# Kernel optimization log

Hardware: AMD Instinct MI355X
Metric: run time of the kernel (lower is better)

## Reference

```python
import jax, jax.numpy as jnp
import numpy as np

T, N, E, D, OUT, L = 12, 10000, 160000, 128, 64, 2


def setup_inputs() -> dict:
    key = jax.random.key(0)
    ks = jax.random.split(key, 8)
    s = 1.0 / np.sqrt(D)
    x = jax.random.normal(ks[0], (T, N, D), jnp.float32)
    hidden_states = jax.random.normal(ks[1], (L, N, D), jnp.float32)
    src = jax.random.randint(ks[2], (E,), 0, N, dtype=jnp.int32)
    dst = jax.random.randint(ks[3], (E,), 0, N, dtype=jnp.int32)
    W_self = jax.random.normal(ks[4], (L, 6, D, D), jnp.float32) * s
    W_neigh = jax.random.normal(ks[5], (L, 6, D, D), jnp.float32) * s
    b = jnp.zeros((L, 6, D), jnp.float32)
    W_out = jax.random.normal(ks[6], (D, OUT), jnp.float32) * s
    b_out = jnp.zeros((OUT,), jnp.float32)
    return dict(x=x, hidden_states=hidden_states, W_self=W_self, W_neigh=W_neigh,
                b=b, W_out=W_out, b_out=b_out, src=src, dst=dst)


def reference(x, hidden_states, W_self, W_neigh, b, W_out, b_out, src, dst):
    n_nodes = x.shape[1]
    deg = jax.ops.segment_sum(jnp.ones_like(dst, jnp.float32), dst, num_segments=n_nodes)
    deg_inv = jnp.where(deg > 0, 1.0 / deg, 0.0)[:, None]  # [N,1]

    def agg(f):  # mean over in-neighbors (DGL update_all copy_u + mean)
        return jax.ops.segment_sum(f[src], dst, num_segments=n_nodes) * deg_inv

    # agg_seq=True: original concatenates all timesteps and does one update_all;
    # mean is per-feature, so this equals per-timestep neighbor means, vmapped.
    hN_all = jax.vmap(agg)(x)  # [T,N,D]

    def net(f, fN, i, Ws, Wn, bl):  # SAGE-mean style message-passing net
        return f @ Ws[i] + fN @ Wn[i] + bl[i]

    def cell(xin, h, hN_x, Ws, Wn, bl):
        if hN_x is None:
            hN_x = agg(xin)
        hN_h = agg(h)
        r = jax.nn.sigmoid(net(xin, hN_x, 0, Ws, Wn, bl) + net(h, hN_h, 1, Ws, Wn, bl))
        u = jax.nn.sigmoid(net(xin, hN_x, 2, Ws, Wn, bl) + net(h, hN_h, 3, Ws, Wn, bl))
        c = jnp.tanh(net(xin, hN_x, 4, Ws, Wn, bl) + net(h, hN_h, 5, Ws, Wn, bl))
        return u * h + (1.0 - u) * c  # note: r*h is dead code in the source

    def step(hidden, inp_t):
        x_t, hN_t = inp_t
        cur, hN = x_t, hN_t
        new_h = []
        for j in range(L):  # small fixed depth
            cur = cell(cur, hidden[j], hN, W_self[j], W_neigh[j], b[j])
            new_h.append(cur)
            hN = None  # h_N only used by first layer (as in source)
        out = cur @ W_out + b_out
        return jnp.stack(new_h), out

    hidden_final, outputs = jax.lax.scan(step, hidden_states, (x, hN_all))
    return outputs, hidden_final
```

## Files before the change

### kernel.cpp

```cpp
#include <hip/hip_runtime.h>

typedef unsigned short u16;
typedef unsigned int   u32;
typedef __attribute__((ext_vector_type(4))) float f32x4;
typedef __attribute__((ext_vector_type(8))) short s16x8;

#define TT 12
#define NN 10000
#define EE 160000
#define DD 128
#define OO 64

__device__ __forceinline__ u16 f2bf(float f) {
  union { float f; u32 u; } x; x.f = f;
  u32 r = x.u + 0x7FFFu + ((x.u >> 16) & 1u);
  return (u16)(r >> 16);
}
__device__ __forceinline__ float bf2f(u16 v) {
  union { u32 u; float f; } x; x.u = (u32)v << 16; return x.f;
}

__global__ __launch_bounds__(256) void prep_kernel(
    const float* __restrict__ x, const float* __restrict__ hs,
    const int* __restrict__ dst,
    const float* __restrict__ Wself, const float* __restrict__ Wneigh,
    const float* __restrict__ b, const float* __restrict__ Wout,
    u16* __restrict__ xb, float* __restrict__ h0f, u16* __restrict__ hb0,
    float* __restrict__ h1f, u16* __restrict__ hb1,
    int* __restrict__ deg, u16* __restrict__ Wp,
    float* __restrict__ biasbuf, u16* __restrict__ WoT,
    int nx4, int nh4half, int E) {
  int gid = blockIdx.x * 256 + threadIdx.x;
  const int NWP = 2 * 256 * 512;
  int cvtEnd  = nx4 + 2 * nh4half;
  int cntEnd  = cvtEnd + E;
  if (gid < nx4) {
    float4 v = *(const float4*)(x + (size_t)gid * 4);
    uint2 p;
    p.x = (u32)f2bf(v.x) | ((u32)f2bf(v.y) << 16);
    p.y = (u32)f2bf(v.z) | ((u32)f2bf(v.w) << 16);
    *(uint2*)(xb + (size_t)gid * 4) = p;
  } else if (gid < cvtEnd) {
    int j = gid - nx4;
    int half = (j >= nh4half);
    int jj = half ? j - nh4half : j;
    float4 v = ((const float4*)hs)[j];
    float* fdst = half ? h1f : h0f;
    u16*   bdst = half ? hb1 : hb0;
    ((float4*)fdst)[jj] = v;
    uint2 p;
    p.x = (u32)f2bf(v.x) | ((u32)f2bf(v.y) << 16);
    p.y = (u32)f2bf(v.z) | ((u32)f2bf(v.w) << 16);
    ((uint2*)bdst)[jj] = p;
  } else if (gid < cntEnd) {
    int e = gid - cvtEnd;
    atomicAdd(&deg[dst[e]], 1);
  } else {
    int pg = gid - cntEnd;
    if (pg < NWP) {
      int j = pg >> 17;
      int rem = pg & 131071;
      int c = rem >> 9;
      int k = rem & 511;
      int seg = k >> 7, kd = k & 127;
      int cc = c & 127;
      int gate = (c < 128) ? (seg < 2 ? 2 : 3) : (seg < 2 ? 4 : 5);
      const float* M = (seg & 1) ? Wneigh : Wself;
      float v = M[((j * 6 + gate) * 128 + kd) * 128 + cc];
      Wp[pg] = f2bf(v);
    } else if (pg < NWP + 64 * 128) {
      int i = pg - NWP;
      int c = i >> 7, k = i & 127;
      WoT[i] = f2bf(Wout[k * OO + c]);
    } else if (pg < NWP + 64 * 128 + 512) {
      int i = pg - NWP - 64 * 128;
      int j = i >> 8, g = (i >> 7) & 1, d = i & 127;
      int g1 = g ? 4 : 2, g2 = g ? 5 : 3;
      biasbuf[i] = b[(j * 6 + g1) * 128 + d] + b[(j * 6 + g2) * 128 + d];
    }
  }
}

__global__ __launch_bounds__(1024) void scan_kernel(const int* __restrict__ deg,
                                                    int* __restrict__ offs,
                                                    float* __restrict__ dinv, int n) {
  __shared__ int lds_deg[10240];
  __shared__ int wsum[16];
  int tid = threadIdx.x;
  for (int i = tid; i < 10240; i += 1024) lds_deg[i] = (i < n) ? deg[i] : 0;
  __syncthreads();
  int base = tid * 10;
  int loc[10];
  int s = 0;
  #pragma unroll
  for (int k = 0; k < 10; ++k) { loc[k] = s; s += lds_deg[base + k]; }
  int lane = tid & 63;
  int incl = s;
  #pragma unroll
  for (int d = 1; d < 64; d <<= 1) {
    int t2 = __shfl_up(incl, d);
    if (lane >= d) incl += t2;
  }
  int wid = tid >> 6;
  if (lane == 63) wsum[wid] = incl;
  __syncthreads();
  int wpre = 0;
  for (int k = 0; k < wid; ++k) wpre += wsum[k];
  int excl = wpre + incl - s;
  #pragma unroll
  for (int k = 0; k < 10; ++k) {
    int idx = base + k;
    if (idx < n) {
      int d0 = lds_deg[idx];
      offs[idx] = excl + loc[k];
      dinv[idx] = (d0 > 0) ? 1.0f / (float)d0 : 0.0f;
    }
  }
  if (tid == 1023) offs[n] = excl + s;
}

__global__ __launch_bounds__(256) void fill_kernel(const int* __restrict__ src,
                                                   const int* __restrict__ dst,
                                                   const int* __restrict__ offs,
                                                   int* __restrict__ cursor,
                                                   int* __restrict__ csr, int E) {
  int e = blockIdx.x * 256 + threadIdx.x;
  if (e >= E) return;
  int d = dst[e];
  int pos = atomicAdd(&cursor[d], 1);
  csr[offs[d] + pos] = src[e] * 64;
}

__device__ __forceinline__ void agg_one(const int* __restrict__ offs,
                                        const int* __restrict__ csr,
                                        const float* __restrict__ dinv,
                                        const u32* __restrict__ S,
                                        u32* __restrict__ O,
                                        int node, int lane) {
  int nu = __builtin_amdgcn_readfirstlane(node);
  int e0 = offs[nu], e1 = offs[nu + 1];
  float di = dinv[nu];
  float xa = 0.f, ya = 0.f, xb_ = 0.f, yb_ = 0.f;
  float xc = 0.f, yc = 0.f, xd = 0.f, yd = 0.f;
  int e = e0;
  for (; e + 8 <= e1; e += 8) {
    int i0 = csr[e],     i1 = csr[e + 1], i2 = csr[e + 2], i3 = csr[e + 3];
    int i4 = csr[e + 4], i5 = csr[e + 5], i6 = csr[e + 6], i7 = csr[e + 7];
    u32 v0 = S[i0 + lane], v1 = S[i1 + lane], v2 = S[i2 + lane], v3 = S[i3 + lane];
    u32 v4 = S[i4 + lane], v5 = S[i5 + lane], v6 = S[i6 + lane], v7 = S[i7 + lane];
    xa  += bf2f((u16)v0) + bf2f((u16)v1);
    ya  += bf2f((u16)(v0 >> 16)) + bf2f((u16)(v1 >> 16));
    xb_ += bf2f((u16)v2) + bf2f((u16)v3);
    yb_ += bf2f((u16)(v2 >> 16)) + bf2f((u16)(v3 >> 16));
    xc  += bf2f((u16)v4) + bf2f((u16)v5);
    yc  += bf2f((u16)(v4 >> 16)) + bf2f((u16)(v5 >> 16));
    xd  += bf2f((u16)v6) + bf2f((u16)v7);
    yd  += bf2f((u16)(v6 >> 16)) + bf2f((u16)(v7 >> 16));
  }
  for (; e + 4 <= e1; e += 4) {
    int i0 = csr[e], i1 = csr[e + 1], i2 = csr[e + 2], i3 = csr[e + 3];
    u32 v0 = S[i0 + lane], v1 = S[i1 + lane], v2 = S[i2 + lane], v3 = S[i3 + lane];
    xa  += bf2f((u16)v0) + bf2f((u16)v1);
    ya  += bf2f((u16)(v0 >> 16)) + bf2f((u16)(v1 >> 16));
    xb_ += bf2f((u16)v2) + bf2f((u16)v3);
    yb_ += bf2f((u16)(v2 >> 16)) + bf2f((u16)(v3 >> 16));
  }
  for (; e < e1; ++e) {
    u32 v = S[csr[e] + lane];
    xa += bf2f((u16)v); ya += bf2f((u16)(v >> 16));
  }
  float sx = ((xa + xb_) + (xc + xd)) * di;
  float sy = ((ya + yb_) + (yc + yd)) * di;
  O[nu * 64 + lane] = (u32)f2bf(sx) | ((u32)f2bf(sy) << 16);
}

__global__ __launch_bounds__(256) void aggs_kernel(const int* __restrict__ offs,
                                                   const int* __restrict__ csr,
                                                   const float* __restrict__ dinv,
                                                   const u16* __restrict__ s,
                                                   u16* __restrict__ o, int N) {
  int node = blockIdx.x * 4 + (threadIdx.x >> 6);
  if (node >= N) return;
  agg_one(offs, csr, dinv, (const u32*)s, (u32*)o, node, threadIdx.x & 63);
}

__global__ __launch_bounds__(256) void aggx_kernel(const int* __restrict__ offs,
                                                   const int* __restrict__ csr,
                                                   const float* __restrict__ dinv,
                                                   const u16* __restrict__ xb,
                                                   u16* __restrict__ axb, int N) {
  int id = blockIdx.x;
  int t, grp;
  if (id < 20000) {
    t = id & 7;
    grp = id >> 3;
  } else {
    int j = id - 20000;
    int slot = j & 7;
    t = 8 + (slot & 3);
    grp = (slot >> 2) * 1250 + (j >> 3);
  }
  int node = grp * 4 + (threadIdx.x >> 6);
  if (node >= N) return;
  size_t yo = (size_t)t * N * 64;
  agg_one(offs, csr, dinv, (const u32*)xb + yo, (u32*)axb + yo, node, threadIdx.x & 63);
}

__global__ __launch_bounds__(256) void aggdual_kernel(const int* __restrict__ offs,
                                                      const int* __restrict__ csr,
                                                      const float* __restrict__ dinv,
                                                      const u16* __restrict__ s0,
                                                      const u16* __restrict__ s1,
                                                      u16* __restrict__ o0,
                                                      u16* __restrict__ o1, int N) {
  int b = blockIdx.x;
  int srcsel = (b >> 2) & 1;
  int idx = (b >> 3) * 4 + (b & 3);
  int node = idx * 4 + (threadIdx.x >> 6);
  if (node >= N) return;
  const u32* S = (const u32*)(srcsel ? s1 : s0);
  u32* O = (u32*)(srcsel ? o1 : o0);
  agg_one(offs, csr, dinv, S, O, node, threadIdx.x & 63);
}

template <int MODE>
__device__ __forceinline__ void cell_body(char* __restrict__ smem, int row0, int tid,
    const u16* __restrict__ s0, const u16* __restrict__ s1,
    const u16* __restrict__ s2, const u16* __restrict__ s3,
    const u16* __restrict__ W, const float* __restrict__ bias,
    float* __restrict__ P,
    const float* __restrict__ hin, float* __restrict__ hout, u16* __restrict__ hbout,
    const u16* __restrict__ WoT, const float* __restrict__ bout,
    float* __restrict__ outp, int N) {
  constexpr int NKC = (MODE == 2) ? 8 : 4;
  u16* As = (u16*)smem;
  u16* Bs = (u16*)(smem + 8192);
  const u16* srcs[4] = {s0, s1, s2, s3};
  int lane = tid & 63, w = tid >> 6;
  int wr = w & 3, wc = w >> 2;

  f32x4 accU[4], accC[4];
  if constexpr (MODE == 1) {
    #pragma unroll
    for (int n = 0; n < 4; ++n) {
      int col = wc * 64 + n * 16 + (lane & 15);
      #pragma unroll
      for (int r = 0; r < 4; ++r) {
        int row = row0 + wr * 16 + (lane >> 4) * 4 + r;
        accU[n][r] = (row < N) ? P[(size_t)row * 256 + col] : 0.f;
        accC[n][r] = (row < N) ? P[(size_t)row * 256 + col + 128] : 0.f;
      }
    }
  } else {
    #pragma unroll
    for (int n = 0; n < 4; ++n) { accU[n] = (f32x4){0,0,0,0}; accC[n] = (f32x4){0,0,0,0}; }
  }

  #pragma unroll
  for (int kc = 0; kc < NKC; ++kc) {
    {
      int r = tid >> 3, k8 = (tid & 7) * 8;
      const u16* sp = srcs[kc >> 1];
      int grow = row0 + r;
      uint4 v = make_uint4(0, 0, 0, 0);
      if (grow < N) v = *(const uint4*)(sp + (size_t)grow * DD + (kc & 1) * 64 + k8);
      int byte = (r * 128 + (tid & 7) * 16) ^ ((r & 7) << 4);
      *(uint4*)((char*)As + byte) = v;
    }
    #pragma unroll
    for (int it = 0; it < 4; ++it) {
      int id = it * 512 + tid;
      int c = id >> 3, k8 = (id & 7) * 8;
      uint4 v = *(const uint4*)(W + c * 512 + kc * 64 + k8);
      int byte = (c * 128 + (id & 7) * 16) ^ ((c & 7) << 4);
      *(uint4*)((char*)Bs + byte) = v;
    }
    __syncthreads();
    #pragma unroll
    for (int ks = 0; ks < 2; ++ks) {
      int arow = wr * 16 + (lane & 15);
      int abyte = (arow * 128 + ks * 64 + (lane >> 4) * 16) ^ ((arow & 7) << 4);
      s16x8 af = *(const s16x8*)((char*)As + abyte);
      #pragma unroll
      for (int n = 0; n < 4; ++n) {
        int cu = wc * 64 + n * 16 + (lane & 15);
        int bub = (cu * 128 + ks * 64 + (lane >> 4) * 16) ^ ((cu & 7) << 4);
        s16x8 bu = *(const s16x8*)((char*)Bs + bub);
        accU[n] = __builtin_amdgcn_mfma_f32_16x16x32_bf16(af, bu, accU[n], 0, 0, 0);
        int cc = cu + 128;
        int bcb = (cc * 128 + ks * 64 + (lane >> 4) * 16) ^ ((cc & 7) << 4);
        s16x8 bc = *(const s16x8*)((char*)Bs + bcb);
        accC[n] = __builtin_amdgcn_mfma_f32_16x16x32_bf16(af, bc, accC[n], 0, 0, 0);
      }
    }
    __syncthreads();
  }

  if constexpr (MODE == 0) {
    #pragma unroll
    for (int n = 0; n < 4; ++n) {
      int col = wc * 64 + n * 16 + (lane & 15);
      #pragma unroll
      for (int r = 0; r < 4; ++r) {
        int row = row0 + wr * 16 + (lane >> 4) * 4 + r;
        if (row < N) {
          P[(size_t)row * 256 + col] = accU[n][r];
          P[(size_t)row * 256 + col + 128] = accC[n][r];
        }
      }
    }
  } else {
    #pragma unroll
    for (int n = 0; n < 4; ++n) {
      int col = wc * 64 + n * 16 + (lane & 15);
      float bu = bias[col], bc = bias[128 + col];
      #pragma unroll
      for (int r = 0; r < 4; ++r) {
        int row = row0 + wr * 16 + (lane >> 4) * 4 + r;
        if (row < N) {
          float u = 1.0f / (1.0f + __expf(-(accU[n][r] + bu)));
          float cg = tanhf(accC[n][r] + bc);
          size_t idx = (size_t)row * DD + col;
          float hn = u * hin[idx] + (1.0f - u) * cg;
          hout[idx] = hn;
          u16 hnb = f2bf(hn);
          hbout[idx] = hnb;
          if constexpr (MODE == 2) {
            int rl = row - row0;
            int hbyte = (rl * 256 + col * 2) ^ ((rl & 7) << 4);
            *(u16*)(smem + hbyte) = hnb;
          }
        }
      }
    }
    if constexpr (MODE == 2) {
      #pragma unroll
      for (int it = 0; it < 2; ++it) {
        int id = it * 512 + tid;
        int c = id >> 4, kc8 = (id & 15) * 8;
        uint4 v = *(const uint4*)(WoT + c * 128 + kc8);
        int byte = (c * 256 + kc8 * 2) ^ ((c & 7) << 4);
        *(uint4*)(smem + 16384 + byte) = v;
      }
      __syncthreads();
      f32x4 ao[2] = {};
      #pragma unroll
      for (int ks = 0; ks < 4; ++ks) {
        int arow = wr * 16 + (lane & 15);
        int abyte = (arow * 256 + ks * 64 + (lane >> 4) * 16) ^ ((arow & 7) << 4);
        s16x8 af = *(const s16x8*)(smem + abyte);
        #pragma unroll
        for (int n = 0; n < 2; ++n) {
          int co = wc * 32 + n * 16 + (lane & 15);
          int bbyte = (co * 256 + ks * 64 + (lane >> 4) * 16) ^ ((co & 7) << 4);
          s16x8 bf = *(const s16x8*)(smem + 16384 + bbyte);
          ao[n] = __builtin_amdgcn_mfma_f32_16x16x32_bf16(af, bf, ao[n], 0, 0, 0);
        }
      }
      #pragma unroll
      for (int n = 0; n < 2; ++n) {
        int co = wc * 32 + n * 16 + (lane & 15);
        float bb = bout[co];
        #pragma unroll
        for (int r = 0; r < 4; ++r) {
          int row = row0 + wr * 16 + (lane >> 4) * 4 + r;
          if (row < N) outp[(size_t)row * OO + co] = ao[n][r] + bb;
        }
      }
    }
  }
}

__global__ __launch_bounds__(512) void pre_kernel(const u16* __restrict__ xb,
                                                  const u16* __restrict__ axb,
                                                  const u16* __restrict__ Wp,
                                                  float* __restrict__ P, int N) {
  __shared__ __align__(16) char smem[40960];
  size_t yo = (size_t)blockIdx.y * N * DD;
  cell_body<0>(smem, blockIdx.x * 64, threadIdx.x, xb + yo, axb + yo, nullptr, nullptr,
               Wp, nullptr, P + (size_t)blockIdx.y * N * 256,
               nullptr, nullptr, nullptr, nullptr, nullptr, nullptr, N);
}

__global__ __launch_bounds__(512) void cell0_kernel(const u16* __restrict__ hb0c,
                                                    const u16* __restrict__ ah0,
                                                    const u16* __restrict__ W,
                                                    const float* __restrict__ bias,
                                                    float* __restrict__ Pt,
                                                    const float* __restrict__ h0in,
                                                    float* __restrict__ h0out,
                                                    u16* __restrict__ hb0out, int N) {
  __shared__ __align__(16) char smem[40960];
  cell_body<1>(smem, blockIdx.x * 64, threadIdx.x, hb0c, ah0, nullptr, nullptr,
               W, bias, Pt, h0in, h0out, hb0out, nullptr, nullptr, nullptr, N);
}

template <int WITHC0>
__global__ __launch_bounds__(512) void step_kernel(const u16* __restrict__ hb0c,
                                                   const u16* __restrict__ ah0,
                                                   const u16* __restrict__ hb1r,
                                                   const u16* __restrict__ ah1,
                                                   const u16* __restrict__ Wp,
                                                   const float* __restrict__ biasbuf,
                                                   float* __restrict__ Pn,
                                                   const float* __restrict__ h1in,
                                                   float* __restrict__ h1out,
                                                   u16* __restrict__ hb1w,
                                                   const float* __restrict__ h0in,
                                                   float* __restrict__ h0out,
                                                   u16* __restrict__ hb0out,
                                                   const u16* __restrict__ WoT,
                                                   const float* __restrict__ bout,
                                                   float* __restrict__ outp, int N) {
  __shared__ __align__(16) char smem[40960];
  int bx = blockIdx.x;
  int role = WITHC0 ? (bx & 1) : 0;
  int row0 = (WITHC0 ? (bx >> 1) : bx) * 64;
  if (role == 0) {
    cell_body<2>(smem, row0, threadIdx.x, hb0c, ah0, hb1r, ah1,
                 Wp + 131072, biasbuf + 256, nullptr,
                 h1in, h1out, hb1w, WoT, bout, outp, N);
  } else {
    cell_body<1>(smem, row0, threadIdx.x, hb0c, ah0, nullptr, nullptr,
                 Wp + 256, biasbuf, Pn,
                 h0in, h0out, hb0out, nullptr, nullptr, nullptr, N);
  }
}

extern "C" void kernel_launch(void* const* d_in, const int* in_sizes, int n_in,
                              void* d_out, int out_size, void* d_ws, size_t ws_size,
                              hipStream_t stream) {
  const float* x      = (const float*)d_in[0];
  const float* hs     = (const float*)d_in[1];
  const float* Wself  = (const float*)d_in[2];
  const float* Wneigh = (const float*)d_in[3];
  const float* b      = (const float*)d_in[4];
  const float* Wout   = (const float*)d_in[5];
  const float* bout   = (const float*)d_in[6];
  const int*   src    = (const int*)d_in[7];
  const int*   dst    = (const int*)d_in[8];
  float* out = (float*)d_out;

  const int N = NN, E = EE, D = DD, T = TT;

  char* ws = (char*)d_ws;
  size_t off = 0;
  auto alloc = [&](size_t bytes) -> void* {
    void* p = ws + off;
    off = (off + bytes + 255) & ~(size_t)255;
    return p;
  };
  int*   deg     = (int*)alloc(N * 4);
  int*   offs    = (int*)alloc((N + 1) * 4);
  int*   cursor  = (int*)alloc(N * 4);
  int*   csr     = (int*)alloc(E * 4);
  float* dinv    = (float*)alloc(N * 4);
  u16*   Wp      = (u16*)alloc(2 * 256 * 512 * 2);
  float* biasbuf = (float*)alloc(512 * 4);
  u16*   WoT     = (u16*)alloc(64 * 128 * 2);
  float* h0A     = (float*)alloc((size_t)N * D * 4);
  float* h0B     = (float*)alloc((size_t)N * D * 4);
  float* h1f     = (float*)alloc((size_t)N * D * 4);
  u16*   hb0A    = (u16*)alloc((size_t)N * D * 2);
  u16*   hb0B    = (u16*)alloc((size_t)N * D * 2);
  u16*   hb1     = (u16*)alloc((size_t)N * D * 2);
  u16*   ah0b    = (u16*)alloc((size_t)N * D * 2);
  u16*   ah1b    = (u16*)alloc((size_t)N * D * 2);
  u16*   xb      = (u16*)alloc((size_t)T * N * D * 2);
  u16*   axb     = (u16*)alloc((size_t)T * N * D * 2);
  float* P       = (float*)alloc((size_t)T * N * 256 * 4);

  float* h0f[2] = {h0A, h0B};
  u16*   hb0[2] = {hb0A, hb0B};
  float* hid0 = out + (size_t)T * N * OO;
  float* hid1 = hid0 + (size_t)N * D;

  hipMemsetAsync(deg, 0, N * 4, stream);
  hipMemsetAsync(cursor, 0, N * 4, stream);
  {
    int nx4 = T * N * D / 4, nh4half = N * D / 4;
    int tot = nx4 + 2 * nh4half + E + (2 * 256 * 512 + 64 * 128 + 512);
    prep_kernel<<<(tot + 255) / 256, 256, 0, stream>>>(
        x, hs, dst, Wself, Wneigh, b, Wout,
        xb, h0A, hb0A, h1f, hb1, deg, Wp, biasbuf, WoT, nx4, nh4half, E);
  }
  scan_kernel<<<1, 1024, 0, stream>>>(deg, offs, dinv, N);
  fill_kernel<<<(E + 255) / 256, 256, 0, stream>>>(src, dst, offs, cursor, csr, E);

  int aggGrid = (N + 3) / 4;
  int mmGrid  = (N + 63) / 64;

  aggx_kernel<<<30000, 256, 0, stream>>>(offs, csr, dinv, xb, axb, N);
  pre_kernel<<<dim3(mmGrid, T), 512, 0, stream>>>(xb, axb, Wp, P, N);
  aggs_kernel<<<aggGrid, 256, 0, stream>>>(offs, csr, dinv, hb0A, ah0b, N);
  cell0_kernel<<<mmGrid, 512, 0, stream>>>(hb0A, ah0b, Wp + 256, biasbuf, P,
                                           h0A, h0B, hb0B, N);

  for (int t = 0; t < T; ++t) {
    u16* cur = hb0[(t + 1) & 1];
    aggdual_kernel<<<2 * aggGrid, 256, 0, stream>>>(offs, csr, dinv, cur, hb1,
                                                    ah0b, ah1b, N);
    if (t < T - 1) {
      float* h0o = (t == T - 2) ? hid0 : h0f[t & 1];
      step_kernel<1><<<2 * mmGrid, 512, 0, stream>>>(
          cur, ah0b, hb1, ah1b, Wp, biasbuf,
          P + (size_t)(t + 1) * N * 256,
          h1f, h1f, hb1,
          h0f[(t + 1) & 1], h0o, hb0[t & 1],
          WoT, bout, out + (size_t)t * N * OO, N);
    } else {
      step_kernel<0><<<mmGrid, 512, 0, stream>>>(
          cur, ah0b, hb1, ah1b, Wp, biasbuf, nullptr,
          h1f, hid1, hb1, nullptr, nullptr, nullptr,
          WoT, bout, out + (size_t)t * N * OO, N);
    }
  }
}
```

Before: 681.0 us.

## Fuse layer-0 input projection into per-step cell kernel, drop precomputed P buffer

Removes the batched pre_kernel that computed x/agg(x) projections for all timesteps into a large fp32 P buffer. The layer-0 cell now runs a full K=512 GEMM over x, agg(x), h and agg(h) each step, so it no longer writes and rereads roughly 123 MB of fp32 partial sums. The prep kernel is also reordered to pack weights first and to convert 8 floats per thread. The trade-off is doubled per-step GEMM K-work for layer 0, which sits on the serial recurrent path, in exchange for removing the P memory traffic.

```diff
diff --git a/kernel.cpp b/kernel.cpp
--- a/kernel.cpp
+++ b/kernel.cpp
@@ -29,34 +29,15 @@
     float* __restrict__ h1f, u16* __restrict__ hb1,
     int* __restrict__ deg, u16* __restrict__ Wp,
     float* __restrict__ biasbuf, u16* __restrict__ WoT,
-    int nx4, int nh4half, int E) {
+    int nx8, int nh8half, int E) {
   int gid = blockIdx.x * 256 + threadIdx.x;
   const int NWP = 2 * 256 * 512;
-  int cvtEnd  = nx4 + 2 * nh4half;
-  int cntEnd  = cvtEnd + E;
-  if (gid < nx4) {
-    float4 v = *(const float4*)(x + (size_t)gid * 4);
-    uint2 p;
-    p.x = (u32)f2bf(v.x) | ((u32)f2bf(v.y) << 16);
-    p.y = (u32)f2bf(v.z) | ((u32)f2bf(v.w) << 16);
-    *(uint2*)(xb + (size_t)gid * 4) = p;
-  } else if (gid < cvtEnd) {
-    int j = gid - nx4;
-    int half = (j >= nh4half);
-    int jj = half ? j - nh4half : j;
-    float4 v = ((const float4*)hs)[j];
-    float* fdst = half ? h1f : h0f;
-    u16*   bdst = half ? hb1 : hb0;
-    ((float4*)fdst)[jj] = v;
-    uint2 p;
-    p.x = (u32)f2bf(v.x) | ((u32)f2bf(v.y) << 16);
-    p.y = (u32)f2bf(v.z) | ((u32)f2bf(v.w) << 16);
-    ((uint2*)bdst)[jj] = p;
-  } else if (gid < cntEnd) {
-    int e = gid - cvtEnd;
-    atomicAdd(&deg[dst[e]], 1);
-  } else {
-    int pg = gid - cntEnd;
+  const int NPACK = NWP + 64 * 128 + 512;
+  int cvtXEnd = NPACK + nx8;
+  int cvtHEnd = cvtXEnd + 2 * nh8half;
+  int cntEnd  = cvtHEnd + E;
+  if (gid < NPACK) {
+    int pg = gid;
     if (pg < NWP) {
       int j = pg >> 17;
       int rem = pg & 131071;
@@ -72,12 +53,41 @@
       int i = pg - NWP;
       int c = i >> 7, k = i & 127;
       WoT[i] = f2bf(Wout[k * OO + c]);
-    } else if (pg < NWP + 64 * 128 + 512) {
+    } else {
       int i = pg - NWP - 64 * 128;
       int j = i >> 8, g = (i >> 7) & 1, d = i & 127;
       int g1 = g ? 4 : 2, g2 = g ? 5 : 3;
       biasbuf[i] = b[(j * 6 + g1) * 128 + d] + b[(j * 6 + g2) * 128 + d];
     }
+  } else if (gid < cvtXEnd) {
+    int i8 = gid - NPACK;
+    float4 va = *(const float4*)(x + (size_t)i8 * 8);
+    float4 vb = *(const float4*)(x + (size_t)i8 * 8 + 4);
+    uint4 p;
+    p.x = (u32)f2bf(va.x) | ((u32)f2bf(va.y) << 16);
+    p.y = (u32)f2bf(va.z) | ((u32)f2bf(va.w) << 16);
+    p.z = (u32)f2bf(vb.x) | ((u32)f2bf(vb.y) << 16);
+    p.w = (u32)f2bf(vb.z) | ((u32)f2bf(vb.w) << 16);
+    *(uint4*)(xb + (size_t)i8 * 8) = p;
+  } else if (gid < cvtHEnd) {
+    int j = gid - cvtXEnd;
+    int half = (j >= nh8half);
+    int jj = half ? j - nh8half : j;
+    float4 va = ((const float4*)hs)[(size_t)j * 2];
+    float4 vb = ((const float4*)hs)[(size_t)j * 2 + 1];
+    float* fdst = half ? h1f : h0f;
+    u16*   bdst = half ? hb1 : hb0;
+    ((float4*)fdst)[(size_t)jj * 2]     = va;
+    ((float4*)fdst)[(size_t)jj * 2 + 1] = vb;
+    uint4 p;
+    p.x = (u32)f2bf(va.x) | ((u32)f2bf(va.y) << 16);
+    p.y = (u32)f2bf(va.z) | ((u32)f2bf(va.w) << 16);
+    p.z = (u32)f2bf(vb.x) | ((u32)f2bf(vb.y) << 16);
+    p.w = (u32)f2bf(vb.z) | ((u32)f2bf(vb.w) << 16);
+    ((uint4*)bdst)[jj] = p;
+  } else if (gid < cntEnd) {
+    int e = gid - cvtHEnd;
+    atomicAdd(&deg[dst[e]], 1);
   }
 }
 
@@ -228,11 +238,9 @@
     const u16* __restrict__ s0, const u16* __restrict__ s1,
     const u16* __restrict__ s2, const u16* __restrict__ s3,
     const u16* __restrict__ W, const float* __restrict__ bias,
-    float* __restrict__ P,
     const float* __restrict__ hin, float* __restrict__ hout, u16* __restrict__ hbout,
     const u16* __restrict__ WoT, const float* __restrict__ bout,
     float* __restrict__ outp, int N) {
-  constexpr int NKC = (MODE == 2) ? 8 : 4;
   u16* As = (u16*)smem;
   u16* Bs = (u16*)(smem + 8192);
   const u16* srcs[4] = {s0, s1, s2, s3};
@@ -240,24 +248,11 @@
   int wr = w & 3, wc = w >> 2;
 
   f32x4 accU[4], accC[4];
-  if constexpr (MODE == 1) {
-    #pragma unroll
-    for (int n = 0; n < 4; ++n) {
-      int col = wc * 64 + n * 16 + (lane & 15);
-      #pragma unroll
-      for (int r = 0; r < 4; ++r) {
-        int row = row0 + wr * 16 + (lane >> 4) * 4 + r;
-        accU[n][r] = (row < N) ? P[(size_t)row * 256 + col] : 0.f;
-        accC[n][r] = (row < N) ? P[(size_t)row * 256 + col + 128] : 0.f;
-      }
-    }
-  } else {
-    #pragma unroll
-    for (int n = 0; n < 4; ++n) { accU[n] = (f32x4){0,0,0,0}; accC[n] = (f32x4){0,0,0,0}; }
-  }
-
-  #pragma unroll
-  for (int kc = 0; kc < NKC; ++kc) {
+  #pragma unroll
+  for (int n = 0; n < 4; ++n) { accU[n] = (f32x4){0,0,0,0}; accC[n] = (f32x4){0,0,0,0}; }
+
+  #pragma unroll
+  for (int kc = 0; kc < 8; ++kc) {
     {
       int r = tid >> 3, k8 = (tid & 7) * 8;
       const u16* sp = srcs[kc >> 1];
@@ -296,113 +291,89 @@
     __syncthreads();
   }
 
-  if constexpr (MODE == 0) {
-    #pragma unroll
-    for (int n = 0; n < 4; ++n) {
-      int col = wc * 64 + n * 16 + (lane & 15);
+  #pragma unroll
+  for (int n = 0; n < 4; ++n) {
+    int col = wc * 64 + n * 16 + (lane & 15);
+    float bu = bias[col], bc = bias[128 + col];
+    #pragma unroll
+    for (int r = 0; r < 4; ++r) {
+      int row = row0 + wr * 16 + (lane >> 4) * 4 + r;
+      if (row < N) {
+        float u = 1.0f / (1.0f + __expf(-(accU[n][r] + bu)));
+        float cg = tanhf(accC[n][r] + bc);
+        size_t idx = (size_t)row * DD + col;
+        float hn = u * hin[idx] + (1.0f - u) * cg;
+        hout[idx] = hn;
+        u16 hnb = f2bf(hn);
+        hbout[idx] = hnb;
+        if constexpr (MODE == 2) {
+          int rl = row - row0;
+          int hbyte = (rl * 256 + col * 2) ^ ((rl & 7) << 4);
+          *(u16*)(smem + hbyte) = hnb;
+        }
+      }
+    }
+  }
+  if constexpr (MODE == 2) {
+    #pragma unroll
+    for (int it = 0; it < 2; ++it) {
+      int id = it * 512 + tid;
+      int c = id >> 4, kc8 = (id & 15) * 8;
+      uint4 v = *(const uint4*)(WoT + c * 128 + kc8);
+      int byte = (c * 256 + kc8 * 2) ^ ((c & 7) << 4);
+      *(uint4*)(smem + 16384 + byte) = v;
+    }
+    __syncthreads();
+    f32x4 ao[2] = {};
+    #pragma unroll
+    for (int ks = 0; ks < 4; ++ks) {
+      int arow = wr * 16 + (lane & 15);
+      int abyte = (arow * 256 + ks * 64 + (lane >> 4) * 16) ^ ((arow & 7) << 4);
+      s16x8 af = *(const s16x8*)(smem + abyte);
+      #pragma unroll
+      for (int n = 0; n < 2; ++n) {
+        int co = wc * 32 + n * 16 + (lane & 15);
+        int bbyte = (co * 256 + ks * 64 + (lane >> 4) * 16) ^ ((co & 7) << 4);
+        s16x8 bf = *(const s16x8*)(smem + 16384 + bbyte);
+        ao[n] = __builtin_amdgcn_mfma_f32_16x16x32_bf16(af, bf, ao[n], 0, 0, 0);
+      }
+    }
+    #pragma unroll
+    for (int n = 0; n < 2; ++n) {
+      int co = wc * 32 + n * 16 + (lane & 15);
+      float bb = bout[co];
       #pragma unroll
       for (int r = 0; r < 4; ++r) {
         int row = row0 + wr * 16 + (lane >> 4) * 4 + r;
-        if (row < N) {
-          P[(size_t)row * 256 + col] = accU[n][r];
-          P[(size_t)row * 256 + col + 128] = accC[n][r];
-        }
+        if (row < N) outp[(size_t)row * OO + co] = ao[n][r] + bb;
       }
     }
-  } else {
-    #pragma unroll
-    for (int n = 0; n < 4; ++n) {
-      int col = wc * 64 + n * 16 + (lane & 15);
-      float bu = bias[col], bc = bias[128 + col];
-      #pragma unroll
-      for (int r = 0; r < 4; ++r) {
-        int row = row0 + wr * 16 + (lane >> 4) * 4 + r;
-        if (row < N) {
-          float u = 1.0f / (1.0f + __expf(-(accU[n][r] + bu)));
-          float cg = tanhf(accC[n][r] + bc);
-          size_t idx = (size_t)row * DD + col;
-          float hn = u * hin[idx] + (1.0f - u) * cg;
-          hout[idx] = hn;
-          u16 hnb = f2bf(hn);
-          hbout[idx] = hnb;
-          if constexpr (MODE == 2) {
-            int rl = row - row0;
-            int hbyte = (rl * 256 + col * 2) ^ ((rl & 7) << 4);
-            *(u16*)(smem + hbyte) = hnb;
-          }
-        }
-      }
-    }
-    if constexpr (MODE == 2) {
-      #pragma unroll
-      for (int it = 0; it < 2; ++it) {
-        int id = it * 512 + tid;
-        int c = id >> 4, kc8 = (id & 15) * 8;
-        uint4 v = *(const uint4*)(WoT + c * 128 + kc8);
-        int byte = (c * 256 + kc8 * 2) ^ ((c & 7) << 4);
-        *(uint4*)(smem + 16384 + byte) = v;
-      }
-      __syncthreads();
-      f32x4 ao[2] = {};
-      #pragma unroll
-      for (int ks = 0; ks < 4; ++ks) {
-        int arow = wr * 16 + (lane & 15);
-        int abyte = (arow * 256 + ks * 64 + (lane >> 4) * 16) ^ ((arow & 7) << 4);
-        s16x8 af = *(const s16x8*)(smem + abyte);
-        #pragma unroll
-        for (int n = 0; n < 2; ++n) {
-          int co = wc * 32 + n * 16 + (lane & 15);
-          int bbyte = (co * 256 + ks * 64 + (lane >> 4) * 16) ^ ((co & 7) << 4);
-          s16x8 bf = *(const s16x8*)(smem + 16384 + bbyte);
-          ao[n] = __builtin_amdgcn_mfma_f32_16x16x32_bf16(af, bf, ao[n], 0, 0, 0);
-        }
-      }
-      #pragma unroll
-      for (int n = 0; n < 2; ++n) {
-        int co = wc * 32 + n * 16 + (lane & 15);
-        float bb = bout[co];
-        #pragma unroll
-        for (int r = 0; r < 4; ++r) {
-          int row = row0 + wr * 16 + (lane >> 4) * 4 + r;
-          if (row < N) outp[(size_t)row * OO + co] = ao[n][r] + bb;
-        }
-      }
-    }
-  }
-}
-
-__global__ __launch_bounds__(512) void pre_kernel(const u16* __restrict__ xb,
-                                                  const u16* __restrict__ axb,
-                                                  const u16* __restrict__ Wp,
-                                                  float* __restrict__ P, int N) {
-  __shared__ __align__(16) char smem[40960];
-  size_t yo = (size_t)blockIdx.y * N * DD;
-  cell_body<0>(smem, blockIdx.x * 64, threadIdx.x, xb + yo, axb + yo, nullptr, nullptr,
-               Wp, nullptr, P + (size_t)blockIdx.y * N * 256,
-               nullptr, nullptr, nullptr, nullptr, nullptr, nullptr, N);
-}
-
-__global__ __launch_bounds__(512) void cell0_kernel(const u16* __restrict__ hb0c,
+  }
+}
+
+__global__ __launch_bounds__(512) void cell0_kernel(const u16* __restrict__ xbt,
+                                                    const u16* __restrict__ axbt,
+                                                    const u16* __restrict__ hb0c,
                                                     const u16* __restrict__ ah0,
                                                     const u16* __restrict__ W,
                                                     const float* __restrict__ bias,
-                                                    float* __restrict__ Pt,
                                                     const float* __restrict__ h0in,
                                                     float* __restrict__ h0out,
                                                     u16* __restrict__ hb0out, int N) {
   __shared__ __align__(16) char smem[40960];
-  cell_body<1>(smem, blockIdx.x * 64, threadIdx.x, hb0c, ah0, nullptr, nullptr,
-               W, bias, Pt, h0in, h0out, hb0out, nullptr, nullptr, nullptr, N);
+  cell_body<3>(smem, blockIdx.x * 64, threadIdx.x, xbt, axbt, hb0c, ah0,
+               W, bias, h0in, h0out, hb0out, nullptr, nullptr, nullptr, N);
 }
 
 template <int WITHC0>
-__global__ __launch_bounds__(512) void step_kernel(const u16* __restrict__ hb0c,
+__global__ __launch_bounds__(512) void step_kernel(const u16* __restrict__ xbn,
+                                                   const u16* __restrict__ axbn,
+                                                   const u16* __restrict__ hb0c,
                                                    const u16* __restrict__ ah0,
                                                    const u16* __restrict__ hb1r,
                                                    const u16* __restrict__ ah1,
                                                    const u16* __restrict__ Wp,
                                                    const float* __restrict__ biasbuf,
-                                                   float* __restrict__ Pn,
                                                    const float* __restrict__ h1in,
                                                    float* __restrict__ h1out,
                                                    u16* __restrict__ hb1w,
@@ -418,11 +389,11 @@
   int row0 = (WITHC0 ? (bx >> 1) : bx) * 64;
   if (role == 0) {
     cell_body<2>(smem, row0, threadIdx.x, hb0c, ah0, hb1r, ah1,
-                 Wp + 131072, biasbuf + 256, nullptr,
+                 Wp + 131072, biasbuf + 256,
                  h1in, h1out, hb1w, WoT, bout, outp, N);
   } else {
-    cell_body<1>(smem, row0, threadIdx.x, hb0c, ah0, nullptr, nullptr,
-                 Wp + 256, biasbuf, Pn,
+    cell_body<3>(smem, row0, threadIdx.x, xbn, axbn, hb0c, ah0,
+                 Wp, biasbuf,
                  h0in, h0out, hb0out, nullptr, nullptr, nullptr, N);
   }
 }
@@ -468,7 +439,6 @@
   u16*   ah1b    = (u16*)alloc((size_t)N * D * 2);
   u16*   xb      = (u16*)alloc((size_t)T * N * D * 2);
   u16*   axb     = (u16*)alloc((size_t)T * N * D * 2);
-  float* P       = (float*)alloc((size_t)T * N * 256 * 4);
 
   float* h0f[2] = {h0A, h0B};
   u16*   hb0[2] = {hb0A, hb0B};
@@ -478,11 +448,12 @@
   hipMemsetAsync(deg, 0, N * 4, stream);
   hipMemsetAsync(cursor, 0, N * 4, stream);
   {
-    int nx4 = T * N * D / 4, nh4half = N * D / 4;
-    int tot = nx4 + 2 * nh4half + E + (2 * 256 * 512 + 64 * 128 + 512);
+    int nx8 = T * N * D / 8, nh8half = N * D / 8;
+    int NPACK = 2 * 256 * 512 + 64 * 128 + 512;
+    int tot = NPACK + nx8 + 2 * nh8half + E;
     prep_kernel<<<(tot + 255) / 256, 256, 0, stream>>>(
         x, hs, dst, Wself, Wneigh, b, Wout,
-        xb, h0A, hb0A, h1f, hb1, deg, Wp, biasbuf, WoT, nx4, nh4half, E);
+        xb, h0A, hb0A, h1f, hb1, deg, Wp, biasbuf, WoT, nx8, nh8half, E);
   }
   scan_kernel<<<1, 1024, 0, stream>>>(deg, offs, dinv, N);
   fill_kernel<<<(E + 255) / 256, 256, 0, stream>>>(src, dst, offs, cursor, csr, E);
@@ -491,9 +462,8 @@
   int mmGrid  = (N + 63) / 64;
 
   aggx_kernel<<<30000, 256, 0, stream>>>(offs, csr, dinv, xb, axb, N);
-  pre_kernel<<<dim3(mmGrid, T), 512, 0, stream>>>(xb, axb, Wp, P, N);
   aggs_kernel<<<aggGrid, 256, 0, stream>>>(offs, csr, dinv, hb0A, ah0b, N);
-  cell0_kernel<<<mmGrid, 512, 0, stream>>>(hb0A, ah0b, Wp + 256, biasbuf, P,
+  cell0_kernel<<<mmGrid, 512, 0, stream>>>(xb, axb, hb0A, ah0b, Wp, biasbuf,
                                            h0A, h0B, hb0B, N);
 
   for (int t = 0; t < T; ++t) {
@@ -503,14 +473,15 @@
     if (t < T - 1) {
       float* h0o = (t == T - 2) ? hid0 : h0f[t & 1];
       step_kernel<1><<<2 * mmGrid, 512, 0, stream>>>(
+          xb + (size_t)(t + 1) * N * D, axb + (size_t)(t + 1) * N * D,
           cur, ah0b, hb1, ah1b, Wp, biasbuf,
-          P + (size_t)(t + 1) * N * 256,
           h1f, h1f, hb1,
           h0f[(t + 1) & 1], h0o, hb0[t & 1],
           WoT, bout, out + (size_t)t * N * OO, N);
     } else {
       step_kernel<0><<<mmGrid, 512, 0, stream>>>(
-          cur, ah0b, hb1, ah1b, Wp, biasbuf, nullptr,
+          nullptr, nullptr,
+          cur, ah0b, hb1, ah1b, Wp, biasbuf,
           h1f, hid1, hb1, nullptr, nullptr, nullptr,
           WoT, bout, out + (size_t)t * N * OO, N);
     }
```

After: 637.6 us. -6.4%, faster.
